# Kernel tuning notes

Measured on AMD Instinct MI355X. Metric: run time of the kernel, lower is better.

The kernel has to match this reference:

```python
import jax, jax.numpy as jnp
import numpy as np

DECAY = 0.99
EPS = 1e-12  # torch F.normalize eps


def setup_inputs() -> dict:
    key = jax.random.key(0)
    ks = jax.random.split(key, 5)
    B, S, H, M = 4, 4096, 1024, 256
    x = jax.random.normal(ks[0], (B, S, H), dtype=jnp.float32)
    Wq = jax.random.normal(ks[1], (M, H), dtype=jnp.float32) * (H ** -0.5)
    Wk = jax.random.normal(ks[2], (M, H), dtype=jnp.float32) * (H ** -0.5)
    Wv = jax.random.normal(ks[3], (M, H), dtype=jnp.float32) * (H ** -0.5)
    # original inits W_out to zeros; use small random weights so the baseline output is non-trivial
    Wo = jax.random.normal(ks[4], (H, M), dtype=jnp.float32) * (M ** -0.5)
    M0 = jnp.zeros((M, M), dtype=jnp.float32)
    return {"x": x, "Wq": Wq, "Wk": Wk, "Wv": Wv, "Wo": Wo, "M0": M0, "chunk_size": 64}


def _l2norm(t):
    return t / jnp.maximum(jnp.linalg.norm(t, axis=-1, keepdims=True), EPS)


def reference(x, Wq, Wk, Wv, Wo, M0, chunk_size):
    B, S, H = x.shape
    m = Wq.shape[0]
    q = jnp.einsum('bsh,mh->bsm', x, Wq)
    k = _l2norm(jnp.einsum('bsh,mh->bsm', x, Wk))
    v = _l2norm(jnp.einsum('bsh,mh->bsm', x, Wv))
    n_chunks = S // chunk_size
    # (n_chunks, B, c, m)
    qc = q.reshape(B, n_chunks, chunk_size, m).transpose(1, 0, 2, 3)
    kc = k.reshape(B, n_chunks, chunk_size, m).transpose(1, 0, 2, 3)
    vc = v.reshape(B, n_chunks, chunk_size, m).transpose(1, 0, 2, 3)
    decay_c = DECAY ** chunk_size
    scale = 1.0 / (B * chunk_size)

    def step(M, qkv):
        qch, kch, vch = qkv
        r = jnp.einsum('bcm,nm->bcn', qch, M)  # q @ M.T
        outer = jnp.einsum('bci,bcj->ij', vch, kch) * scale
        return decay_c * M + outer, r

    _, rs = jax.lax.scan(step, M0, (qc, kc, vc))  # rs: (n_chunks, B, c, m)
    retrieved = rs.transpose(1, 0, 2, 3).reshape(B, S, m)
    return jnp.einsum('bsm,hm->bsh', retrieved, Wo)
```

## Files before the change

kernel.cpp:

```cpp
#include <hip/hip_runtime.h>
#include <math.h>

#define BB 4
#define SS 4096
#define HH 1024
#define MM 256
#define CHUNK 64
#define NCHUNK 64
#define ROWS (BB*SS)
#define QKV_LD 768
#define DECAY_F 0.99

typedef unsigned short u16;
typedef __attribute__((ext_vector_type(8))) short bf16x8;
typedef __attribute__((ext_vector_type(8))) unsigned short u16x8;
typedef __attribute__((ext_vector_type(4))) float f32x4;

__device__ inline u16 f2b(float f) {
  union { float f; unsigned u; } v; v.f = f;
  unsigned r = v.u + 0x7FFF + ((v.u >> 16) & 1);
  return (u16)(r >> 16);
}
__device__ inline float b2f(u16 h) {
  union { unsigned u; float f; } v; v.u = ((unsigned)h) << 16; return v.f;
}

__device__ inline void gload16(const void* g, void* l) {
  __builtin_amdgcn_global_load_lds(
      (const __attribute__((address_space(1))) unsigned int*)g,
      (__attribute__((address_space(3))) unsigned int*)l, 16, 0, 0);
}

__global__ __launch_bounds__(256) void cast_x_kernel(const float* __restrict__ src,
                                                     u16* __restrict__ dst) {
  int i = blockIdx.x * 256 + threadIdx.x;
  float4 v = reinterpret_cast<const float4*>(src)[i];
  ushort4 o;
  o.x = f2b(v.x); o.y = f2b(v.y); o.z = f2b(v.z); o.w = f2b(v.w);
  reinterpret_cast<ushort4*>(dst)[i] = o;
}

__global__ __launch_bounds__(256) void cast_w_kernel(const float* __restrict__ Wq,
                                                     const float* __restrict__ Wk,
                                                     const float* __restrict__ Wv,
                                                     const float* __restrict__ Wo,
                                                     u16* __restrict__ Wqkv_b,
                                                     u16* __restrict__ Wo_b) {
  int b = blockIdx.x, which = b >> 8;
  int i = ((b & 255) << 8) + threadIdx.x;
  const float* src = which == 0 ? Wq : which == 1 ? Wk : which == 2 ? Wv : Wo;
  u16* dst = which < 3 ? Wqkv_b + which * (MM * HH) : Wo_b;
  float4 v = reinterpret_cast<const float4*>(src)[i];
  ushort4 o;
  o.x = f2b(v.x); o.y = f2b(v.y); o.z = f2b(v.z); o.w = f2b(v.w);
  reinterpret_cast<ushort4*>(dst)[i] = o;
}

#define M_STD_BF16 0
#define M_STD_F32  1
#define M_OUTER    2
#define M_RETR     3

template<int MODE>
__global__ __launch_bounds__(256) void gemm128(const u16* __restrict__ A,
                                               const u16* __restrict__ Bg,
                                               void* __restrict__ Cv,
                                               int K, int lda, int ldb, int ldc,
                                               float scale) {
  __shared__ bf16x8 As[3][512];
  __shared__ bf16x8 Bs[3][512];
  const int tid = threadIdx.x, lane = tid & 63, wv = tid >> 6;
  const int wr = wv >> 1, wc = wv & 1;
  const int t = (MODE == M_OUTER || MODE == M_RETR) ? blockIdx.z : 0;

  int bx, by;
  if (MODE == M_STD_BF16 || MODE == M_STD_F32) {
    int gx = gridDim.x;
    int nwg = gx * gridDim.y;
    int lin = blockIdx.y * gx + blockIdx.x;
    int chunk = nwg >> 3;
    int orig = (lin & 7) * chunk + (lin >> 3);
    bx = orig % gx; by = orig / gx;
  } else { bx = blockIdx.x; by = blockIdx.y; }

  const int row0 = by * 128;
  const int col0 = bx * 128;
  const int NK = K >> 5;
  const u16* Bbase = (MODE == M_RETR) ? (Bg + (size_t)t * (MM * MM)) : Bg;

  auto stage = [&](int ks, int buf) {
    int koff;
    if (MODE == M_OUTER) koff = ((ks >> 1) << 12) + t * CHUNK + ((ks & 1) << 5);
    else                 koff = ks << 5;
#pragma unroll
    for (int j = 0; j < 2; ++j) {
      int m = j * 4 + wv;
      int rf = m * 16 + (lane & 15);
      size_t arow;
      if (MODE == M_RETR)
        arow = (size_t)(2 * by + (rf >> 6)) * SS + (size_t)t * CHUNK + (rf & 63);
      else
        arow = (size_t)(row0 + rf);
      const u16* ga = A + arow * (size_t)lda + koff + ((lane >> 4) << 3);
      gload16(ga, &As[buf][m * 64]);
      const u16* gb = Bbase + (size_t)(col0 + rf) * ldb + koff + ((lane >> 4) << 3);
      gload16(gb, &Bs[buf][m * 64]);
    }
  };

  f32x4 acc[4][4] = {};
  stage(0, 0);
  stage(1, 1);
  int rb = 0, sb = 2;
  for (int ks = 0; ks < NK; ++ks) {
    if (ks + 1 < NK) asm volatile("s_waitcnt vmcnt(4)" ::: "memory");
    else             asm volatile("s_waitcnt vmcnt(0)" ::: "memory");
    __builtin_amdgcn_s_barrier();
    if (ks + 2 < NK) stage(ks + 2, sb);
    bf16x8 af[4], bfr[4];
#pragma unroll
    for (int m = 0; m < 4; ++m) af[m] = As[rb][(wr * 4 + m) * 64 + lane];
#pragma unroll
    for (int n = 0; n < 4; ++n) bfr[n] = Bs[rb][(wc * 4 + n) * 64 + lane];
#pragma unroll
    for (int m = 0; m < 4; ++m)
#pragma unroll
      for (int n = 0; n < 4; ++n)
        acc[m][n] = __builtin_amdgcn_mfma_f32_16x16x32_bf16(af[m], bfr[n], acc[m][n], 0, 0, 0);
    rb = (rb == 2) ? 0 : rb + 1;
    sb = (sb == 2) ? 0 : sb + 1;
  }

  const int r4 = (lane >> 4) << 2;
  const int cc = lane & 15;
#pragma unroll
  for (int m = 0; m < 4; ++m)
#pragma unroll
    for (int n = 0; n < 4; ++n)
#pragma unroll
      for (int r = 0; r < 4; ++r) {
        int lr = wr * 64 + m * 16 + r4 + r;
        int lc = wc * 64 + n * 16 + cc;
        float vv = acc[m][n][r];
        if (MODE == M_STD_BF16) {
          ((u16*)Cv)[(size_t)(row0 + lr) * ldc + col0 + lc] = f2b(vv);
        } else if (MODE == M_STD_F32) {
          ((float*)Cv)[(size_t)(row0 + lr) * ldc + col0 + lc] = vv;
        } else if (MODE == M_OUTER) {
          ((float*)Cv)[(size_t)t * (MM * MM) + (size_t)(row0 + lr) * MM + col0 + lc] = vv * scale;
        } else {
          size_t rowg = (size_t)(2 * by + (lr >> 6)) * SS + (size_t)t * CHUNK + (lr & 63);
          ((u16*)Cv)[rowg * MM + col0 + lc] = f2b(vv);
        }
      }
}

__global__ __launch_bounds__(256) void l2normT_kernel(const u16* __restrict__ qkv,
                                                      u16* __restrict__ kT,
                                                      u16* __restrict__ vT) {
  __shared__ u16 T[256][72];
  __shared__ float ps[64][4];
  __shared__ float inv[64];
  const int tid = threadIdx.x;
  const int q = tid >> 6, rl = tid & 63;
  const int row0 = blockIdx.x * 64;
#pragma unroll 1
  for (int seg = 0; seg < 2; ++seg) {
    u16* dstT = seg ? vT : kT;
    const int segbase = 256 + seg * 256;
    float ss = 0.f;
#pragma unroll
    for (int i = 0; i < 8; ++i) {
      u16x8 v = *reinterpret_cast<const u16x8*>(
          qkv + (size_t)(row0 + rl) * QKV_LD + segbase + q * 64 + i * 8);
#pragma unroll
      for (int e = 0; e < 8; ++e) {
        float f = b2f(v[e]);
        ss += f * f;
        T[q * 64 + i * 8 + e][rl] = v[e];
      }
    }
    ps[rl][q] = ss;
    __syncthreads();
    if (tid < 64) {
      float s = ps[tid][0] + ps[tid][1] + ps[tid][2] + ps[tid][3];
      inv[tid] = 1.0f / fmaxf(sqrtf(s), 1e-12f);
    }
    __syncthreads();
#pragma unroll
    for (int p = 0; p < 8; ++p) {
      int c = p * 32 + q * 8 + (rl >> 3);
      int r0 = (rl & 7) * 8;
      u16x8 val = *reinterpret_cast<const u16x8*>(&T[c][r0]);
      u16x8 o;
#pragma unroll
      for (int e = 0; e < 8; ++e) o[e] = f2b(b2f(val[e]) * inv[r0 + e]);
      *reinterpret_cast<u16x8*>(dstT + (size_t)c * ROWS + row0 + r0) = o;
    }
    __syncthreads();
  }
}

__global__ __launch_bounds__(256) void prefix_kernel(const float* __restrict__ outer,
                                                     const float* __restrict__ M0,
                                                     u16* __restrict__ Mprev_b,
                                                     float decay_c) {
  int ij = blockIdx.x * 256 + threadIdx.x;
  float run = M0[ij];
  float pre[8];
#pragma unroll
  for (int d = 0; d < 8; ++d) pre[d] = outer[(size_t)d * (MM * MM) + ij];
#pragma unroll 1
  for (int tb = 0; tb < NCHUNK; tb += 8) {
#pragma unroll
    for (int d = 0; d < 8; ++d) {
      int tc = tb + d;
      float o = pre[d];
      if (tb + 8 < NCHUNK) pre[d] = outer[(size_t)(tc + 8) * (MM * MM) + ij];
      Mprev_b[(size_t)tc * (MM * MM) + ij] = f2b(run);
      run = decay_c * run + o;
    }
  }
}

extern "C" void kernel_launch(void* const* d_in, const int* in_sizes, int n_in,
                              void* d_out, int out_size, void* d_ws, size_t ws_size,
                              hipStream_t stream) {
  const float* x  = (const float*)d_in[0];
  const float* Wq = (const float*)d_in[1];
  const float* Wk = (const float*)d_in[2];
  const float* Wv = (const float*)d_in[3];
  const float* Wo = (const float*)d_in[4];
  const float* M0 = (const float*)d_in[5];
  float* out = (float*)d_out;

  char* ws = (char*)d_ws;
  u16*   xb      = (u16*)(ws);
  u16*   qkv_b   = (u16*)(ws + 33554432);
  u16*   Wqkv_b  = (u16*)(ws + 58720256);
  u16*   Wo_b    = (u16*)(ws + 60293120);
  u16*   kT      = (u16*)(ws);
  u16*   vT      = (u16*)(ws + 8388608);
  float* outer   = (float*)(ws + 16777216);
  u16*   Mprev_b = (u16*)(ws + 8388608);
  u16*   r_b     = (u16*)(ws);

  const float scale   = 1.0f / (BB * CHUNK);
  const float decay_c = (float)pow(DECAY_F, (double)CHUNK);
  dim3 blk(256);

  cast_x_kernel<<<(ROWS * HH / 4) / 256, blk, 0, stream>>>(x, xb);
  cast_w_kernel<<<1024, blk, 0, stream>>>(Wq, Wk, Wv, Wo, Wqkv_b, Wo_b);
  gemm128<M_STD_BF16><<<dim3(QKV_LD / 128, ROWS / 128), blk, 0, stream>>>(
      xb, Wqkv_b, qkv_b, HH, HH, HH, QKV_LD, 0.f);
  l2normT_kernel<<<ROWS / 64, blk, 0, stream>>>(qkv_b, kT, vT);
  gemm128<M_OUTER><<<dim3(2, 2, NCHUNK), blk, 0, stream>>>(
      vT, kT, outer, MM, ROWS, ROWS, MM, scale);
  prefix_kernel<<<(MM * MM) / 256, blk, 0, stream>>>(outer, M0, Mprev_b, decay_c);
  gemm128<M_RETR><<<dim3(2, 2, NCHUNK), blk, 0, stream>>>(
      qkv_b, Mprev_b, r_b, MM, QKV_LD, MM, MM, 0.f);
  gemm128<M_STD_F32><<<dim3(HH / 128, ROWS / 128), blk, 0, stream>>>(
      r_b, Wo_b, out, MM, MM, MM, HH, 0.f);
}
```

Before: 153.2 us.

## Fuse x bf16 cast into QKV GEMM and switch to register-staged 512-thread GEMM

Drops the separate kernel that cast x to bf16; the QKV GEMM now reads fp32 x directly and converts it in registers before writing to LDS, which removes a full write and re-read of the 32 MB bf16 copy of x. All GEMMs move from direct global-to-LDS async loads with triple buffering to register-staged double buffering, using 512-thread blocks of 8 waves, each wave computing a 64x32 tile. The workspace layout is reshuffled to match. The trade-off is twice the fp32 read traffic for x in the QKV GEMM and a loss of the global_load_lds async path, so latency hiding now relies on register prefetch.

Result: no change. 150.3 us (-1.9%).

```diff
diff --git a/kernel.cpp b/kernel.cpp
--- a/kernel.cpp
+++ b/kernel.cpp
@@ -23,21 +23,6 @@
 }
 __device__ inline float b2f(u16 h) {
   union { unsigned u; float f; } v; v.u = ((unsigned)h) << 16; return v.f;
-}
-
-__device__ inline void gload16(const void* g, void* l) {
-  __builtin_amdgcn_global_load_lds(
-      (const __attribute__((address_space(1))) unsigned int*)g,
-      (__attribute__((address_space(3))) unsigned int*)l, 16, 0, 0);
-}
-
-__global__ __launch_bounds__(256) void cast_x_kernel(const float* __restrict__ src,
-                                                     u16* __restrict__ dst) {
-  int i = blockIdx.x * 256 + threadIdx.x;
-  float4 v = reinterpret_cast<const float4*>(src)[i];
-  ushort4 o;
-  o.x = f2b(v.x); o.y = f2b(v.y); o.z = f2b(v.z); o.w = f2b(v.w);
-  reinterpret_cast<ushort4*>(dst)[i] = o;
 }
 
 __global__ __launch_bounds__(256) void cast_w_kernel(const float* __restrict__ Wq,
@@ -56,25 +41,25 @@
   reinterpret_cast<ushort4*>(dst)[i] = o;
 }
 
-#define M_STD_BF16 0
-#define M_STD_F32  1
-#define M_OUTER    2
-#define M_RETR     3
+#define M_QKV   0
+#define M_OUT   1
+#define M_OUTER 2
+#define M_RETR  3
 
 template<int MODE>
-__global__ __launch_bounds__(256) void gemm128(const u16* __restrict__ A,
-                                               const u16* __restrict__ Bg,
-                                               void* __restrict__ Cv,
-                                               int K, int lda, int ldb, int ldc,
-                                               float scale) {
-  __shared__ bf16x8 As[3][512];
-  __shared__ bf16x8 Bs[3][512];
+__global__ __launch_bounds__(512, 4) void gemm_v2(const void* __restrict__ Ap,
+                                                  const u16* __restrict__ Bp,
+                                                  void* __restrict__ Cv,
+                                                  float scale) {
+  constexpr int NK = (MODE == M_QKV) ? 32 : 8;
+  __shared__ bf16x8 As[2][512];
+  __shared__ bf16x8 Bs[2][512];
   const int tid = threadIdx.x, lane = tid & 63, wv = tid >> 6;
-  const int wr = wv >> 1, wc = wv & 1;
-  const int t = (MODE == M_OUTER || MODE == M_RETR) ? blockIdx.z : 0;
+  const int wr = wv >> 2, wc = wv & 3;
+  const int t64 = (MODE == M_OUTER || MODE == M_RETR) ? blockIdx.z : 0;
 
   int bx, by;
-  if (MODE == M_STD_BF16 || MODE == M_STD_F32) {
+  if (MODE == M_QKV || MODE == M_OUT) {
     int gx = gridDim.x;
     int nwg = gx * gridDim.y;
     int lin = blockIdx.y * gx + blockIdx.x;
@@ -85,50 +70,81 @@
 
   const int row0 = by * 128;
   const int col0 = bx * 128;
-  const int NK = K >> 5;
-  const u16* Bbase = (MODE == M_RETR) ? (Bg + (size_t)t * (MM * MM)) : Bg;
-
-  auto stage = [&](int ks, int buf) {
-    int koff;
-    if (MODE == M_OUTER) koff = ((ks >> 1) << 12) + t * CHUNK + ((ks & 1) << 5);
-    else                 koff = ks << 5;
-#pragma unroll
-    for (int j = 0; j < 2; ++j) {
-      int m = j * 4 + wv;
-      int rf = m * 16 + (lane & 15);
-      size_t arow;
-      if (MODE == M_RETR)
-        arow = (size_t)(2 * by + (rf >> 6)) * SS + (size_t)t * CHUNK + (rf & 63);
-      else
-        arow = (size_t)(row0 + rf);
-      const u16* ga = A + arow * (size_t)lda + koff + ((lane >> 4) << 3);
-      gload16(ga, &As[buf][m * 64]);
-      const u16* gb = Bbase + (size_t)(col0 + rf) * ldb + koff + ((lane >> 4) << 3);
-      gload16(gb, &Bs[buf][m * 64]);
-    }
-  };
-
-  f32x4 acc[4][4] = {};
-  stage(0, 0);
-  stage(1, 1);
-  int rb = 0, sb = 2;
-  for (int ks = 0; ks < NK; ++ks) {
-    if (ks + 1 < NK) asm volatile("s_waitcnt vmcnt(4)" ::: "memory");
-    else             asm volatile("s_waitcnt vmcnt(0)" ::: "memory");
-    __builtin_amdgcn_s_barrier();
-    if (ks + 2 < NK) stage(ks + 2, sb);
-    bf16x8 af[4], bfr[4];
-#pragma unroll
-    for (int m = 0; m < 4; ++m) af[m] = As[rb][(wr * 4 + m) * 64 + lane];
-#pragma unroll
-    for (int n = 0; n < 4; ++n) bfr[n] = Bs[rb][(wc * 4 + n) * 64 + lane];
+  const int ar  = ((tid >> 6) << 4) | (tid & 15);
+  const int kof = ((tid >> 4) & 3) << 3;
+
+  auto aoff = [&](int ks) -> size_t {
+    if (MODE == M_QKV)  return (size_t)(row0 + ar) * HH + ks * 32 + kof;
+    if (MODE == M_OUT)  return (size_t)(row0 + ar) * MM + ks * 32 + kof;
+    if (MODE == M_OUTER) return (size_t)(row0 + ar) * ROWS + (ks >> 1) * SS +
+                                t64 * CHUNK + ((ks & 1) << 5) + kof;
+     return ((size_t)(2 * by + (ar >> 6)) * SS + t64 * CHUNK + (ar & 63)) * QKV_LD +
+                        ks * 32 + kof;
+  };
+  auto boff = [&](int ks) -> size_t {
+    if (MODE == M_QKV)  return (size_t)(col0 + ar) * HH + ks * 32 + kof;
+    if (MODE == M_OUT)  return (size_t)(col0 + ar) * MM + ks * 32 + kof;
+    if (MODE == M_OUTER) return (size_t)(col0 + ar) * ROWS + (ks >> 1) * SS +
+                                t64 * CHUNK + ((ks & 1) << 5) + kof;
+     return (size_t)t64 * (MM * MM) + (size_t)(col0 + ar) * MM + ks * 32 + kof;
+  };
+
+  float4 fA0a, fA0b, fA1a, fA1b;
+  u16x8 rA0, rA1, rB0, rB1;
+
+  auto loadA = [&](int ks, int p) {
+    if (MODE == M_QKV) {
+      const float* pa = (const float*)Ap + aoff(ks);
+      if (p == 0) { fA0a = *(const float4*)pa; fA0b = *(const float4*)(pa + 4); }
+      else        { fA1a = *(const float4*)pa; fA1b = *(const float4*)(pa + 4); }
+    } else {
+      const u16* pa = (const u16*)Ap + aoff(ks);
+      if (p == 0) rA0 = *(const u16x8*)pa; else rA1 = *(const u16x8*)pa;
+    }
+  };
+  auto loadB = [&](int ks, int p) {
+    const u16* pb = Bp + boff(ks);
+    if (p == 0) rB0 = *(const u16x8*)pb; else rB1 = *(const u16x8*)pb;
+  };
+  auto writeLDS = [&](int buf, int p) {
+    u16x8 ha;
+    if (MODE == M_QKV) {
+      float4 fa = p ? fA1a : fA0a, fb = p ? fA1b : fA0b;
+      ha[0] = f2b(fa.x); ha[1] = f2b(fa.y); ha[2] = f2b(fa.z); ha[3] = f2b(fa.w);
+      ha[4] = f2b(fb.x); ha[5] = f2b(fb.y); ha[6] = f2b(fb.z); ha[7] = f2b(fb.w);
+    } else ha = p ? rA1 : rA0;
+    *reinterpret_cast<u16x8*>(&As[buf][tid]) = ha;
+    *reinterpret_cast<u16x8*>(&Bs[buf][tid]) = p ? rB1 : rB0;
+  };
+
+  f32x4 acc[4][2] = {};
+  auto compute = [&](int buf) {
+    bf16x8 af[4], bfv[2];
+#pragma unroll
+    for (int m = 0; m < 4; ++m) af[m] = As[buf][(wr * 4 + m) * 64 + lane];
+#pragma unroll
+    for (int n = 0; n < 2; ++n) bfv[n] = Bs[buf][(wc * 2 + n) * 64 + lane];
 #pragma unroll
     for (int m = 0; m < 4; ++m)
 #pragma unroll
-      for (int n = 0; n < 4; ++n)
-        acc[m][n] = __builtin_amdgcn_mfma_f32_16x16x32_bf16(af[m], bfr[n], acc[m][n], 0, 0, 0);
-    rb = (rb == 2) ? 0 : rb + 1;
-    sb = (sb == 2) ? 0 : sb + 1;
+      for (int n = 0; n < 2; ++n)
+        acc[m][n] = __builtin_amdgcn_mfma_f32_16x16x32_bf16(af[m], bfv[n], acc[m][n], 0, 0, 0);
+  };
+
+  loadA(0, 0); loadB(0, 0);
+  loadA(1, 1); loadB(1, 1);
+  writeLDS(0, 0);
+  for (int ks0 = 0; ; ks0 += 2) {
+    if (ks0 + 2 < NK) { loadA(ks0 + 2, 0); loadB(ks0 + 2, 0); }
+    __syncthreads();
+    compute(0);
+    if (ks0 + 1 >= NK) break;
+    writeLDS(1, 1);
+    if (ks0 + 3 < NK) { loadA(ks0 + 3, 1); loadB(ks0 + 3, 1); }
+    __syncthreads();
+    compute(1);
+    if (ks0 + 2 >= NK) break;
+    writeLDS(0, 0);
   }
 
   const int r4 = (lane >> 4) << 2;
@@ -136,20 +152,20 @@
 #pragma unroll
   for (int m = 0; m < 4; ++m)
 #pragma unroll
-    for (int n = 0; n < 4; ++n)
+    for (int n = 0; n < 2; ++n)
 #pragma unroll
       for (int r = 0; r < 4; ++r) {
         int lr = wr * 64 + m * 16 + r4 + r;
-        int lc = wc * 64 + n * 16 + cc;
+        int lc = wc * 32 + n * 16 + cc;
         float vv = acc[m][n][r];
-        if (MODE == M_STD_BF16) {
-          ((u16*)Cv)[(size_t)(row0 + lr) * ldc + col0 + lc] = f2b(vv);
-        } else if (MODE == M_STD_F32) {
-          ((float*)Cv)[(size_t)(row0 + lr) * ldc + col0 + lc] = vv;
+        if (MODE == M_QKV) {
+          ((u16*)Cv)[(size_t)(row0 + lr) * QKV_LD + col0 + lc] = f2b(vv);
+        } else if (MODE == M_OUT) {
+          ((float*)Cv)[(size_t)(row0 + lr) * HH + col0 + lc] = vv;
         } else if (MODE == M_OUTER) {
-          ((float*)Cv)[(size_t)t * (MM * MM) + (size_t)(row0 + lr) * MM + col0 + lc] = vv * scale;
+          ((float*)Cv)[(size_t)t64 * (MM * MM) + (size_t)(row0 + lr) * MM + col0 + lc] = vv * scale;
         } else {
-          size_t rowg = (size_t)(2 * by + (lr >> 6)) * SS + (size_t)t * CHUNK + (lr & 63);
+          size_t rowg = (size_t)(2 * by + (lr >> 6)) * SS + (size_t)t64 * CHUNK + (lr & 63);
           ((u16*)Cv)[rowg * MM + col0 + lc] = f2b(vv);
         }
       }
@@ -235,30 +251,28 @@
   float* out = (float*)d_out;
 
   char* ws = (char*)d_ws;
-  u16*   xb      = (u16*)(ws);
-  u16*   qkv_b   = (u16*)(ws + 33554432);
+  u16*   qkv_b   = (u16*)(ws);
+  u16*   kT      = (u16*)(ws + 25165824);
+  u16*   vT      = (u16*)(ws + 33554432);
+  float* outer   = (float*)(ws + 41943040);
+  u16*   Mprev_b = (u16*)(ws + 25165824);
+  u16*   r_b     = (u16*)(ws + 33554432);
   u16*   Wqkv_b  = (u16*)(ws + 58720256);
   u16*   Wo_b    = (u16*)(ws + 60293120);
-  u16*   kT      = (u16*)(ws);
-  u16*   vT      = (u16*)(ws + 8388608);
-  float* outer   = (float*)(ws + 16777216);
-  u16*   Mprev_b = (u16*)(ws + 8388608);
-  u16*   r_b     = (u16*)(ws);
 
   const float scale   = 1.0f / (BB * CHUNK);
   const float decay_c = (float)pow(DECAY_F, (double)CHUNK);
-  dim3 blk(256);
-
-  cast_x_kernel<<<(ROWS * HH / 4) / 256, blk, 0, stream>>>(x, xb);
+  dim3 blk512(512), blk(256);
+
   cast_w_kernel<<<1024, blk, 0, stream>>>(Wq, Wk, Wv, Wo, Wqkv_b, Wo_b);
-  gemm128<M_STD_BF16><<<dim3(QKV_LD / 128, ROWS / 128), blk, 0, stream>>>(
-      xb, Wqkv_b, qkv_b, HH, HH, HH, QKV_LD, 0.f);
+  gemm_v2<M_QKV><<<dim3(QKV_LD / 128, ROWS / 128), blk512, 0, stream>>>(
+      x, Wqkv_b, qkv_b, 0.f);
   l2normT_kernel<<<ROWS / 64, blk, 0, stream>>>(qkv_b, kT, vT);
-  gemm128<M_OUTER><<<dim3(2, 2, NCHUNK), blk, 0, stream>>>(
-      vT, kT, outer, MM, ROWS, ROWS, MM, scale);
+  gemm_v2<M_OUTER><<<dim3(2, 2, NCHUNK), blk512, 0, stream>>>(
+      vT, kT, outer, scale);
   prefix_kernel<<<(MM * MM) / 256, blk, 0, stream>>>(outer, M0, Mprev_b, decay_c);
-  gemm128<M_RETR><<<dim3(2, 2, NCHUNK), blk, 0, stream>>>(
-      qkv_b, Mprev_b, r_b, MM, QKV_LD, MM, MM, 0.f);
-  gemm128<M_STD_F32><<<dim3(HH / 128, ROWS / 128), blk, 0, stream>>>(
-      r_b, Wo_b, out, MM, MM, MM, HH, 0.f);
-}
+  gemm_v2<M_RETR><<<dim3(2, 2, NCHUNK), blk512, 0, stream>>>(
+      qkv_b, Mprev_b, r_b, 0.f);
+  gemm_v2<M_OUT><<<dim3(HH / 128, ROWS / 128), blk512, 0, stream>>>(
+      r_b, Wo_b, out, 0.f);
+}
```

## Use 256x256-tile 8-wave GEMM with interleaved prefetch for projection GEMMs

Applied to the files above, without the earlier changes.

Replaces the 128x128 GEMM for the QKV projection and the output projection with a new 256x256-tile, 512-thread kernel. It uses a K-step of 64, double-buffered LDS, prefetch split into four parts interleaved with MFMA clusters, and s_setprio around the MFMA clusters. The aim is more data reuse per tile and better overlap of global loads with matrix math. The cost is higher register and LDS pressure and fewer workgroups: the QKV GEMM grid is only 3x64 blocks. The workspace aliasing of Mprev and r_b is also swapped.

After: 140.5 us, median of 2. 8.3% less time.

```diff
diff --git a/kernel.cpp b/kernel.cpp
--- a/kernel.cpp
+++ b/kernel.cpp
@@ -56,33 +56,128 @@
   reinterpret_cast<ushort4*>(dst)[i] = o;
 }
 
-#define M_STD_BF16 0
-#define M_STD_F32  1
-#define M_OUTER    2
-#define M_RETR     3
+template<int OUT_BF16>
+__global__ __launch_bounds__(512, 2) void gemm256(const u16* __restrict__ A,
+                                                  const u16* __restrict__ B,
+                                                  void* __restrict__ Cv,
+                                                  int K, int lda, int ldb, int ldc) {
+  __shared__ bf16x8 LD[2][2][2][16][64];
+  const int tid = threadIdx.x, lane = tid & 63, wv = tid >> 6;
+  const int wr = wv >> 2, wc = wv & 3;
+
+  const int gx = gridDim.x;
+  const int nwg = gx * gridDim.y;
+  const int lin = blockIdx.y * gx + blockIdx.x;
+  const int chunk = nwg >> 3;
+  const int orig = (lin & 7) * chunk + (lin >> 3);
+  const int bx = orig % gx, by = orig / gx;
+  const int row0 = by * 256, col0 = bx * 256;
+  const int NT = K >> 6;
+
+  const int fr = lane & 15;
+  const int kg = (lane >> 4) << 3;
+
+  auto stage2 = [&](int kt, int db, int part) {
+    const int ab = part >> 1;
+    const int j = part & 1;
+    const int tile = wv + (j << 3);
+    const u16* base = ab ? B : A;
+    const int ld = ab ? ldb : lda;
+    const int rc0 = ab ? col0 : row0;
+    const u16* g = base + (size_t)(rc0 + tile * 16 + fr) * ld + kt * 64 + kg;
+    gload16(g,      &LD[db][ab][0][tile][0]);
+    gload16(g + 32, &LD[db][ab][1][tile][0]);
+  };
+
+  bf16x8 aq[4][2], bq[4][2];
+  auto readAquad = [&](int db, int h) {
+#pragma unroll
+    for (int i = 0; i < 4; ++i)
+#pragma unroll
+      for (int s = 0; s < 2; ++s)
+        aq[i][s] = LD[db][0][s][wr * 8 + h * 4 + i][lane];
+  };
+  auto readB2 = [&](int db, int nh) {
+#pragma unroll
+    for (int j = 0; j < 2; ++j)
+#pragma unroll
+      for (int s = 0; s < 2; ++s)
+        bq[nh * 2 + j][s] = LD[db][1][s][wc * 4 + nh * 2 + j][lane];
+  };
+
+  f32x4 acc[8][4] = {};
+  auto cluster = [&](int h, int nh) {
+#pragma unroll
+    for (int i = 0; i < 4; ++i)
+#pragma unroll
+      for (int j = 0; j < 2; ++j)
+#pragma unroll
+        for (int s = 0; s < 2; ++s)
+          acc[h * 4 + i][nh * 2 + j] = __builtin_amdgcn_mfma_f32_16x16x32_bf16(
+              aq[i][s], bq[nh * 2 + j][s], acc[h * 4 + i][nh * 2 + j], 0, 0, 0);
+  };
+
+  stage2(0, 0, 0); stage2(0, 0, 1); stage2(0, 0, 2); stage2(0, 0, 3);
+
+  for (int kt = 0; kt < NT; ++kt) {
+    const int db = kt & 1;
+    const bool pf = (kt + 1 < NT);
+    if (pf) stage2(kt + 1, db ^ 1, 0);
+    if (pf) asm volatile("s_waitcnt vmcnt(2)" ::: "memory");
+    else    asm volatile("s_waitcnt vmcnt(0)" ::: "memory");
+    __builtin_amdgcn_s_barrier();
+    asm volatile("" ::: "memory");
+    readAquad(db, 0);
+    readB2(db, 0);
+    __builtin_amdgcn_s_setprio(1); cluster(0, 0); __builtin_amdgcn_s_setprio(0);
+    __builtin_amdgcn_s_barrier();
+    readB2(db, 1);
+    if (pf) stage2(kt + 1, db ^ 1, 1);
+    __builtin_amdgcn_s_barrier();
+    __builtin_amdgcn_s_setprio(1); cluster(0, 1); __builtin_amdgcn_s_setprio(0);
+    __builtin_amdgcn_s_barrier();
+    readAquad(db, 1);
+    if (pf) stage2(kt + 1, db ^ 1, 2);
+    __builtin_amdgcn_s_barrier();
+    __builtin_amdgcn_s_setprio(1); cluster(1, 0); __builtin_amdgcn_s_setprio(0);
+    __builtin_amdgcn_s_barrier();
+    if (pf) stage2(kt + 1, db ^ 1, 3);
+    __builtin_amdgcn_s_barrier();
+    __builtin_amdgcn_s_setprio(1); cluster(1, 1); __builtin_amdgcn_s_setprio(0);
+    __builtin_amdgcn_s_barrier();
+  }
+
+  const int r4 = (lane >> 4) << 2;
+  const int cc = lane & 15;
+#pragma unroll
+  for (int mi = 0; mi < 8; ++mi)
+#pragma unroll
+    for (int nj = 0; nj < 4; ++nj)
+#pragma unroll
+      for (int r = 0; r < 4; ++r) {
+        int lr = wr * 128 + mi * 16 + r4 + r;
+        int lc = wc * 64 + nj * 16 + cc;
+        float vv = acc[mi][nj][r];
+        if (OUT_BF16) ((u16*)Cv)[(size_t)(row0 + lr) * ldc + col0 + lc] = f2b(vv);
+        else          ((float*)Cv)[(size_t)(row0 + lr) * ldc + col0 + lc] = vv;
+      }
+}
+
+#define M_OUTER 2
+#define M_RETR  3
 
 template<int MODE>
 __global__ __launch_bounds__(256) void gemm128(const u16* __restrict__ A,
                                                const u16* __restrict__ Bg,
                                                void* __restrict__ Cv,
-                                               int K, int lda, int ldb, int ldc,
+                                               int K, int lda, int ldb,
                                                float scale) {
   __shared__ bf16x8 As[3][512];
   __shared__ bf16x8 Bs[3][512];
   const int tid = threadIdx.x, lane = tid & 63, wv = tid >> 6;
   const int wr = wv >> 1, wc = wv & 1;
-  const int t = (MODE == M_OUTER || MODE == M_RETR) ? blockIdx.z : 0;
-
-  int bx, by;
-  if (MODE == M_STD_BF16 || MODE == M_STD_F32) {
-    int gx = gridDim.x;
-    int nwg = gx * gridDim.y;
-    int lin = blockIdx.y * gx + blockIdx.x;
-    int chunk = nwg >> 3;
-    int orig = (lin & 7) * chunk + (lin >> 3);
-    bx = orig % gx; by = orig / gx;
-  } else { bx = blockIdx.x; by = blockIdx.y; }
-
+  const int t = blockIdx.z;
+  const int bx = blockIdx.x, by = blockIdx.y;
   const int row0 = by * 128;
   const int col0 = bx * 128;
   const int NK = K >> 5;
@@ -116,6 +211,7 @@
     if (ks + 1 < NK) asm volatile("s_waitcnt vmcnt(4)" ::: "memory");
     else             asm volatile("s_waitcnt vmcnt(0)" ::: "memory");
     __builtin_amdgcn_s_barrier();
+    asm volatile("" ::: "memory");
     if (ks + 2 < NK) stage(ks + 2, sb);
     bf16x8 af[4], bfr[4];
 #pragma unroll
@@ -142,11 +238,7 @@
         int lr = wr * 64 + m * 16 + r4 + r;
         int lc = wc * 64 + n * 16 + cc;
         float vv = acc[m][n][r];
-        if (MODE == M_STD_BF16) {
-          ((u16*)Cv)[(size_t)(row0 + lr) * ldc + col0 + lc] = f2b(vv);
-        } else if (MODE == M_STD_F32) {
-          ((float*)Cv)[(size_t)(row0 + lr) * ldc + col0 + lc] = vv;
-        } else if (MODE == M_OUTER) {
+        if (MODE == M_OUTER) {
           ((float*)Cv)[(size_t)t * (MM * MM) + (size_t)(row0 + lr) * MM + col0 + lc] = vv * scale;
         } else {
           size_t rowg = (size_t)(2 * by + (lr >> 6)) * SS + (size_t)t * CHUNK + (lr & 63);
@@ -242,23 +334,23 @@
   u16*   kT      = (u16*)(ws);
   u16*   vT      = (u16*)(ws + 8388608);
   float* outer   = (float*)(ws + 16777216);
-  u16*   Mprev_b = (u16*)(ws + 8388608);
-  u16*   r_b     = (u16*)(ws);
+  u16*   Mprev_b = (u16*)(ws);
+  u16*   r_b     = (u16*)(ws + 8388608);
 
   const float scale   = 1.0f / (BB * CHUNK);
   const float decay_c = (float)pow(DECAY_F, (double)CHUNK);
-  dim3 blk(256);
+  dim3 blk(256), blk512(512);
 
   cast_x_kernel<<<(ROWS * HH / 4) / 256, blk, 0, stream>>>(x, xb);
   cast_w_kernel<<<1024, blk, 0, stream>>>(Wq, Wk, Wv, Wo, Wqkv_b, Wo_b);
-  gemm128<M_STD_BF16><<<dim3(QKV_LD / 128, ROWS / 128), blk, 0, stream>>>(
-      xb, Wqkv_b, qkv_b, HH, HH, HH, QKV_LD, 0.f);
+  gemm256<1><<<dim3(QKV_LD / 256, ROWS / 256), blk512, 0, stream>>>(
+      xb, Wqkv_b, qkv_b, HH, HH, HH, QKV_LD);
   l2normT_kernel<<<ROWS / 64, blk, 0, stream>>>(qkv_b, kT, vT);
   gemm128<M_OUTER><<<dim3(2, 2, NCHUNK), blk, 0, stream>>>(
-      vT, kT, outer, MM, ROWS, ROWS, MM, scale);
+      vT, kT, outer, MM, ROWS, ROWS, scale);
   prefix_kernel<<<(MM * MM) / 256, blk, 0, stream>>>(outer, M0, Mprev_b, decay_c);
   gemm128<M_RETR><<<dim3(2, 2, NCHUNK), blk, 0, stream>>>(
-      qkv_b, Mprev_b, r_b, MM, QKV_LD, MM, MM, 0.f);
-  gemm128<M_STD_F32><<<dim3(HH / 128, ROWS / 128), blk, 0, stream>>>(
-      r_b, Wo_b, out, MM, MM, MM, HH, 0.f);
-}
+      qkv_b, Mprev_b, r_b, MM, QKV_LD, MM, 0.f);
+  gemm256<0><<<dim3(HH / 256, ROWS / 256), blk512, 0, stream>>>(
+      r_b, Wo_b, out, MM, MM, MM, HH);
+}
```
